# Optimization experiments

Measured on AMD Instinct MI355X. Metric: run time of the kernel, lower is better.

Reference implementation:

```python
import jax, jax.numpy as jnp
import numpy as np

B, S, E, HD = 32, 1024, 768, 64
NUM_IMAGE_PATCHES = 49


def setup_inputs() -> dict:
    key = jax.random.key(0)
    ks = jax.random.split(key, 9)
    w = 0.02
    return {
        "decoder_sequence": jax.random.normal(ks[0], (B, S, E), dtype=jnp.float32),
        "Wq": jax.random.normal(ks[1], (E, HD), dtype=jnp.float32) * w,
        "bq": jnp.zeros((HD,), dtype=jnp.float32),
        "Wk": jax.random.normal(ks[2], (E, HD), dtype=jnp.float32) * w,
        "bk": jnp.zeros((HD,), dtype=jnp.float32),
        "Wv": jax.random.normal(ks[3], (E, HD), dtype=jnp.float32) * w,
        "bv": jnp.zeros((HD,), dtype=jnp.float32),
        "input_sequence_length": 975,
        "padding_mask": jax.random.randint(ks[4], (B, 1, S), 0, 2).astype(bool),
    }


def reference(decoder_sequence, Wq, bq, Wk, bk, Wv, bv, input_sequence_length, padding_mask):
    # single-head projections: [B,S,E] @ [E,HD] -> [B,S,HD]
    Q = decoder_sequence @ Wq + bq
    K = decoder_sequence @ Wk + bk
    V = decoder_sequence @ Wv + bv

    scores = jnp.einsum('bid,bjd->bij', Q, K) / jnp.sqrt(jnp.float32(HD))

    # mask: image-patch rows (i < 49) fully unmasked; text region is causal
    # (mask[49:,49:] = triu(-inf, diag=1)), i.e. -inf where i >= 49 and j > i.
    i = jnp.arange(S)[:, None]
    j = jnp.arange(S)[None, :]
    causal_bad = (i >= NUM_IMAGE_PATCHES) & (j > i)  # [S,S]
    scores = jnp.where(causal_bad[None, :, :], -jnp.inf, scores)

    # padding mask on keys, broadcast over queries: [B,1,S] -> [B,S,S]
    scores = jnp.where(padding_mask, -jnp.inf, scores)

    A = jax.nn.softmax(scores, axis=-1)
    H = jnp.einsum('bij,bjd->bid', A, V)
    return H
```

## Files before the change

### kernel.cpp

```cpp
#include <hip/hip_runtime.h>
#include <stdint.h>
#include <stddef.h>


typedef __attribute__((ext_vector_type(8))) short bf16x8;
typedef __attribute__((ext_vector_type(4))) float f32x4;

#define NIP 49
#define QSCALE 0.18033688011112042f

#define GLDS16(g, l)                                      \
  __builtin_amdgcn_global_load_lds(                       \
      (const __attribute__((address_space(1))) void*)(g), \
      (__attribute__((address_space(3))) void*)(l), 16, 0, 0)

__device__ __forceinline__ short f2b(float f) {
  union { float f; uint32_t u; } c; c.f = f;
  uint32_t u = c.u;
  uint32_t r = (u + 0x7fffu + ((u >> 16) & 1u)) >> 16;
  return (short)(uint16_t)r;
}

__global__ __launch_bounds__(256) void wt_kernel(
    const float* __restrict__ Wq, const float* __restrict__ Wk,
    const float* __restrict__ Wv, short* __restrict__ Wt) {
  int idx = blockIdx.x * 256 + threadIdx.x;
  int n = idx / 768;
  int k = idx - n * 768;
  const float* W = (n < 64) ? Wq : (n < 128) ? Wk : Wv;
  Wt[idx] = f2b(W[(size_t)k * 64 + (n & 63)]);
}

__global__ __launch_bounds__(256, 3) void proj_kernel(
    const float* __restrict__ X, const float* __restrict__ bq,
    const float* __restrict__ bk, const float* __restrict__ bv,
    const short* __restrict__ Wt, short* __restrict__ Qg,
    short* __restrict__ Kg, short* __restrict__ Vt) {
  const int tid = threadIdx.x;
  const int wid = tid >> 6, lane = tid & 63;
  const int l15 = lane & 15, q4 = lane >> 4;
  const int r0 = (blockIdx.x * 4 + wid) * 16;

  const float* xp = X + (size_t)(r0 + l15) * 768 + q4 * 8;
  const short* wp = Wt + (size_t)l15 * 768 + q4 * 8;

  f32x4 acc[12];
#pragma unroll
  for (int c = 0; c < 12; ++c) acc[c] = (f32x4){0.f, 0.f, 0.f, 0.f};

  float4 a0 = *(const float4*)(xp);
  float4 a1 = *(const float4*)(xp + 4);

  for (int k0 = 0; k0 < 768; k0 += 32) {
    bf16x8 a;
    a[0] = f2b(a0.x); a[1] = f2b(a0.y); a[2] = f2b(a0.z); a[3] = f2b(a0.w);
    a[4] = f2b(a1.x); a[5] = f2b(a1.y); a[6] = f2b(a1.z); a[7] = f2b(a1.w);
    if (k0 + 32 < 768) {
      a0 = *(const float4*)(xp + k0 + 32);
      a1 = *(const float4*)(xp + k0 + 36);
    }
#pragma unroll
    for (int c = 0; c < 12; ++c) {
      bf16x8 bw = *(const bf16x8*)(wp + (size_t)c * 16 * 768 + k0);
      acc[c] = __builtin_amdgcn_mfma_f32_16x16x32_bf16(a, bw, acc[c], 0, 0, 0);
    }
  }

  const int b = r0 >> 10, s0 = r0 & 1023;
#pragma unroll
  for (int c = 0; c < 12; ++c) {
    const int mtx = c >> 2;
    const int h = (c & 3) * 16 + l15;
    if (mtx < 2) {
      const float bias = (mtx == 0 ? bq : bk)[h];
      short* op = (mtx == 0) ? Qg : Kg;
#pragma unroll
      for (int rr = 0; rr < 4; ++rr) {
        int row = r0 + q4 * 4 + rr;
        float v = acc[c][rr] + bias;
        if (mtx == 0) v *= QSCALE;
        op[(size_t)row * 64 + h] = f2b(v);
      }
    } else {
      const float bias = bv[h];
      short4 sv;
      sv.x = f2b(acc[c][0] + bias); sv.y = f2b(acc[c][1] + bias);
      sv.z = f2b(acc[c][2] + bias); sv.w = f2b(acc[c][3] + bias);
      *(short4*)(Vt + ((size_t)(b * 64 + h) << 10) + s0 + q4 * 4) = sv;
    }
  }
}

__global__ __launch_bounds__(256, 2) void attn_kernel(
    const short* __restrict__ Qg, const short* __restrict__ Kg,
    const short* __restrict__ Vt, const int* __restrict__ pad,
    float* __restrict__ out) {
  __shared__ short lK[2][2][128][32];
  __shared__ short lV[2][4][64][32];
  __shared__ short lP[4][16][68];
  __shared__ short lOnes[16][32];

  const int b = blockIdx.x;
  const int level = blockIdx.y;
  const int t = (level == 0) ? 0 : 16 - level;
  const int tid = threadIdx.x;
  const int wid = tid >> 6, lane = tid & 63;
  const int l15 = lane & 15, q4 = lane >> 4;
  const int qs = t * 64;
  const size_t base = (size_t)b * 1024;
  const int nkt = (t == 0) ? 8 : (t / 2 + 1);

  {
    int i0 = tid, i1 = tid + 256;
    ((short*)lOnes)[i0] = ((i0 >> 5) == 0) ? (short)0x3F80 : (short)0;
    if (i1 < 512) ((short*)lOnes)[i1] = ((i1 >> 5) == 0) ? (short)0x3F80 : (short)0;
  }

  const short* qrow = Qg + (base + qs + wid * 16 + l15) * 64;
  bf16x8 aq0 = *(const bf16x8*)(qrow + q4 * 8);
  bf16x8 aq1 = *(const bf16x8*)(qrow + 32 + q4 * 8);

  const int sr = lane >> 2, sc = (lane & 3) * 8;
  auto wlds_tile = [&](int buf, int kt) {
    const int kb = kt * 128;
#pragma unroll
    for (int i = 0; i < 4; ++i) {
      const int dh = i & 1, krow = wid * 32 + (i >> 1) * 16;
      GLDS16(Kg + (base + kb + krow + sr) * 64 + dh * 32 + sc,
             &lK[buf][dh][krow][0]);
    }
#pragma unroll
    for (int kq = 0; kq < 4; ++kq) {
      GLDS16(Vt + ((size_t)(b * 64 + wid * 16 + sr) << 10) + kb + kq * 32 + sc,
             &lV[buf][kq][wid * 16][0]);
    }
  };
  int pc[8];
  auto pload = [&](int kt) {
#pragma unroll
    for (int c = 0; c < 8; ++c) pc[c] = pad[base + kt * 128 + c * 16 + l15];
  };

  pload(0);
  wlds_tile(0, 0);
  __syncthreads();

  f32x4 o[5];
#pragma unroll
  for (int c = 0; c < 5; ++c) o[c] = (f32x4){0.f, 0.f, 0.f, 0.f};

  for (int kt = 0; kt < nkt; ++kt) {
    const int cur = kt & 1;
    const int kb = kt * 128;
    float padm[8];
#pragma unroll
    for (int c = 0; c < 8; ++c) padm[c] = (pc[c] != 0) ? 0.f : 1.f;
    if (kt + 1 < nkt) {
      wlds_tile(cur ^ 1, kt + 1);
      pload(kt + 1);
    }

    f32x4 s4[8];
#pragma unroll
    for (int c = 0; c < 8; ++c) {
      s4[c] = (f32x4){0.f, 0.f, 0.f, 0.f};
      bf16x8 b0 = *(const bf16x8*)&lK[cur][0][c * 16 + l15][q4 * 8];
      s4[c] = __builtin_amdgcn_mfma_f32_16x16x32_bf16(aq0, b0, s4[c], 0, 0, 0);
      bf16x8 b1 = *(const bf16x8*)&lK[cur][1][c * 16 + l15][q4 * 8];
      s4[c] = __builtin_amdgcn_mfma_f32_16x16x32_bf16(aq1, b1, s4[c], 0, 0, 0);
    }

    const bool diag = (t == 0) ? (kt == 0) : (kt == nkt - 1);
    const bool img = (t == 0 && kt > 0);
    float p[8][4];
#pragma unroll
    for (int rr = 0; rr < 4; ++rr) {
      const int qi = qs + wid * 16 + q4 * 4 + rr;
#pragma unroll
      for (int c = 0; c < 8; ++c) {
        float pv = exp2f(fminf(s4[c][rr], 80.f)) * padm[c];
        if (diag) {
          int j = kb + c * 16 + l15;
          if (qi >= NIP && j > qi) pv = 0.f;
        }
        if (img && qi >= NIP) pv = 0.f;
        p[c][rr] = pv;
      }
    }

#pragma unroll
    for (int half = 0; half < 2; ++half) {
#pragma unroll
      for (int rr = 0; rr < 4; ++rr)
#pragma unroll
        for (int c = 0; c < 4; ++c)
          lP[wid][q4 * 4 + rr][c * 16 + l15] = f2b(p[half * 4 + c][rr]);
      bf16x8 ap0 = *(const bf16x8*)&lP[wid][l15][q4 * 8];
      bf16x8 ap1 = *(const bf16x8*)&lP[wid][l15][32 + q4 * 8];
      const int kq0 = half * 2, kq1 = half * 2 + 1;
#pragma unroll
      for (int c = 0; c < 5; ++c) {
        bf16x8 b0 = (c < 4) ? *(const bf16x8*)&lV[cur][kq0][c * 16 + l15][q4 * 8]
                            : *(const bf16x8*)&lOnes[l15][q4 * 8];
        o[c] = __builtin_amdgcn_mfma_f32_16x16x32_bf16(ap0, b0, o[c], 0, 0, 0);
        bf16x8 b1 = (c < 4) ? *(const bf16x8*)&lV[cur][kq1][c * 16 + l15][q4 * 8]
                            : *(const bf16x8*)&lOnes[l15][q4 * 8];
        o[c] = __builtin_amdgcn_mfma_f32_16x16x32_bf16(ap1, b1, o[c], 0, 0, 0);
      }
    }
    __syncthreads();
  }

#pragma unroll
  for (int rr = 0; rr < 4; ++rr) {
    float l = __shfl(o[4][rr], lane & 48, 64);
    const float inv = (l > 0.f) ? 1.0f / l : 0.f;
    const size_t row = base + qs + wid * 16 + q4 * 4 + rr;
#pragma unroll
    for (int c = 0; c < 4; ++c)
      out[row * 64 + c * 16 + l15] = o[c][rr] * inv;
  }
}

extern "C" void kernel_launch(void* const* d_in, const int* in_sizes, int n_in,
                              void* d_out, int out_size, void* d_ws, size_t ws_size,
                              hipStream_t stream) {
  const float* X  = (const float*)d_in[0];
  const float* Wq = (const float*)d_in[1];
  const float* bq = (const float*)d_in[2];
  const float* Wk = (const float*)d_in[3];
  const float* bk = (const float*)d_in[4];
  const float* Wv = (const float*)d_in[5];
  const float* bv = (const float*)d_in[6];
  const int* pad  = (const int*)d_in[8];
  float* out = (float*)d_out;

  short* Qg = (short*)d_ws;
  short* Kg = Qg + 32768 * 64;
  short* Vt = Kg + 32768 * 64;
  short* Wt = Vt + 32768 * 64;

  wt_kernel<<<576, 256, 0, stream>>>(Wq, Wk, Wv, Wt);
  proj_kernel<<<512, 256, 0, stream>>>(X, bq, bk, bv, Wt, Qg, Kg, Vt);
  attn_kernel<<<dim3(32, 16), 256, 0, stream>>>(Qg, Kg, Vt, pad, out);
}
```

Before: 245.6 us.

## Pre-swizzle weights into MFMA fragment order and software-pipeline projection loads

Result: faster. 221.9 us (-9.7%).

```diff
diff --git a/kernel.cpp b/kernel.cpp
--- a/kernel.cpp
+++ b/kernel.cpp
@@ -23,18 +23,22 @@
 
 __global__ __launch_bounds__(256) void wt_kernel(
     const float* __restrict__ Wq, const float* __restrict__ Wk,
-    const float* __restrict__ Wv, short* __restrict__ Wt) {
+    const float* __restrict__ Wv, short* __restrict__ Wf) {
   int idx = blockIdx.x * 256 + threadIdx.x;
-  int n = idx / 768;
-  int k = idx - n * 768;
+  int e = idx & 7;
+  int lane = (idx >> 3) & 63;
+  int rem = idx >> 9;
+  int c = rem % 12, kc = rem / 12;
+  int k = kc * 32 + (lane >> 4) * 8 + e;
+  int n = c * 16 + (lane & 15);
   const float* W = (n < 64) ? Wq : (n < 128) ? Wk : Wv;
-  Wt[idx] = f2b(W[(size_t)k * 64 + (n & 63)]);
-}
-
-__global__ __launch_bounds__(256, 3) void proj_kernel(
+  Wf[idx] = f2b(W[(size_t)k * 64 + (n & 63)]);
+}
+
+__global__ __launch_bounds__(256, 2) void proj_kernel(
     const float* __restrict__ X, const float* __restrict__ bq,
     const float* __restrict__ bk, const float* __restrict__ bv,
-    const short* __restrict__ Wt, short* __restrict__ Qg,
+    const short* __restrict__ Wf, short* __restrict__ Qg,
     short* __restrict__ Kg, short* __restrict__ Vt) {
   const int tid = threadIdx.x;
   const int wid = tid >> 6, lane = tid & 63;
@@ -42,28 +46,43 @@
   const int r0 = (blockIdx.x * 4 + wid) * 16;
 
   const float* xp = X + (size_t)(r0 + l15) * 768 + q4 * 8;
-  const short* wp = Wt + (size_t)l15 * 768 + q4 * 8;
+  const short* wf = Wf + lane * 8;
 
   f32x4 acc[12];
 #pragma unroll
   for (int c = 0; c < 12; ++c) acc[c] = (f32x4){0.f, 0.f, 0.f, 0.f};
 
-  float4 a0 = *(const float4*)(xp);
-  float4 a1 = *(const float4*)(xp + 4);
-
-  for (int k0 = 0; k0 < 768; k0 += 32) {
+  float4 xa[3][2];
+  bf16x8 bfr[2][12];
+
+  xa[0][0] = *(const float4*)(xp);
+  xa[0][1] = *(const float4*)(xp + 4);
+  xa[1][0] = *(const float4*)(xp + 32);
+  xa[1][1] = *(const float4*)(xp + 36);
+#pragma unroll
+  for (int c = 0; c < 12; ++c)
+    bfr[0][c] = *(const bf16x8*)(wf + c * 512);
+
+#pragma unroll
+  for (int kc = 0; kc < 24; ++kc) {
+    if (kc + 1 < 24) {
+#pragma unroll
+      for (int c = 0; c < 12; ++c)
+        bfr[(kc + 1) & 1][c] =
+            *(const bf16x8*)(wf + (kc + 1) * 6144 + c * 512);
+    }
+    if (kc + 2 < 24) {
+      xa[(kc + 2) % 3][0] = *(const float4*)(xp + (kc + 2) * 32);
+      xa[(kc + 2) % 3][1] = *(const float4*)(xp + (kc + 2) * 32 + 4);
+    }
+    const float4 a0 = xa[kc % 3][0], a1 = xa[kc % 3][1];
     bf16x8 a;
     a[0] = f2b(a0.x); a[1] = f2b(a0.y); a[2] = f2b(a0.z); a[3] = f2b(a0.w);
     a[4] = f2b(a1.x); a[5] = f2b(a1.y); a[6] = f2b(a1.z); a[7] = f2b(a1.w);
-    if (k0 + 32 < 768) {
-      a0 = *(const float4*)(xp + k0 + 32);
-      a1 = *(const float4*)(xp + k0 + 36);
-    }
-#pragma unroll
-    for (int c = 0; c < 12; ++c) {
-      bf16x8 bw = *(const bf16x8*)(wp + (size_t)c * 16 * 768 + k0);
-      acc[c] = __builtin_amdgcn_mfma_f32_16x16x32_bf16(a, bw, acc[c], 0, 0, 0);
-    }
+#pragma unroll
+    for (int c = 0; c < 12; ++c)
+      acc[c] = __builtin_amdgcn_mfma_f32_16x16x32_bf16(a, bfr[kc & 1][c],
+                                                       acc[c], 0, 0, 0);
   }
 
   const int b = r0 >> 10, s0 = r0 & 1023;
@@ -238,9 +257,9 @@
   short* Qg = (short*)d_ws;
   short* Kg = Qg + 32768 * 64;
   short* Vt = Kg + 32768 * 64;
-  short* Wt = Vt + 32768 * 64;
-
-  wt_kernel<<<576, 256, 0, stream>>>(Wq, Wk, Wv, Wt);
-  proj_kernel<<<512, 256, 0, stream>>>(X, bq, bk, bv, Wt, Qg, Kg, Vt);
+  short* Wf = Vt + 32768 * 64;
+
+  wt_kernel<<<576, 256, 0, stream>>>(Wq, Wk, Wv, Wf);
+  proj_kernel<<<512, 256, 0, stream>>>(X, bq, bk, bv, Wf, Qg, Kg, Vt);
   attn_kernel<<<dim3(32, 16), 256, 0, stream>>>(Qg, Kg, Vt, pad, out);
 }
```
